# Kernel tuning notes

Hardware: AMD Instinct MI355X
Metric: run time of the kernel (lower is better)

## Reference

```python
import jax, jax.numpy as jnp
import numpy as np

R_RAYS = 65536
S_PER_RAY = 128
N_TOTAL = R_RAYS * S_PER_RAY


def setup_inputs() -> dict:
    key = jax.random.key(0)
    k1, k2, k3, k4 = jax.random.split(key, 4)
    sigmas = jax.random.uniform(k1, (N_TOTAL,), dtype=jnp.float32) * 2.0  # densities >= 0
    rgbs = jax.random.uniform(k2, (N_TOTAL, 3), dtype=jnp.float32)
    deltas = jax.random.uniform(k3, (N_TOTAL,), dtype=jnp.float32) * 0.01 + 1e-3
    ts = jax.random.uniform(k4, (N_TOTAL,), dtype=jnp.float32) * 6.0 + 0.1
    ray_idx = jnp.arange(R_RAYS, dtype=jnp.int32)
    rays_a = jnp.stack([ray_idx, ray_idx * S_PER_RAY,
                        jnp.full((R_RAYS,), S_PER_RAY, dtype=jnp.int32)], axis=1)
    return {"sigmas": sigmas, "rgbs": rgbs, "deltas": deltas, "ts": ts,
            "rays_a": rays_a, "T_threshold": 1e-4}


def reference(sigmas, rgbs, deltas, ts, rays_a, T_threshold):
    R = rays_a.shape[0]
    N = sigmas.shape[0]
    S_max = int(jnp.max(rays_a[:, 2]))  # max samples per ray (concrete)

    offs = jnp.arange(S_max, dtype=rays_a.dtype)
    valid = offs[None, :] < rays_a[:, 2, None]              # [R, S] prefix mask
    idx = jnp.where(valid, rays_a[:, 1, None] + offs[None, :], N - 1)  # [R, S]

    a = 1.0 - jnp.exp(-sigmas[idx] * deltas[idx])           # [R, S] alphas

    # Sequential transmittance recurrence with early-exit (T set to 0 once below threshold)
    def step(T, xs):
        a_s, v_s = xs                                        # [R], [R]
        alive = (T > T_threshold) & v_s
        w = jnp.where(alive, a_s * T, 0.0)
        T = jnp.where(alive, T * (1.0 - a_s), 0.0)
        return T, (w, alive)

    T0 = jnp.ones((R,), sigmas.dtype)
    _, (wT, aliveT) = jax.lax.scan(step, T0, (a.T, valid.T))
    w = wT.T                                                 # [R, S] weights
    alive = aliveT.T

    op_n = jnp.sum(w, axis=1)                                # [R]
    dep_n = jnp.sum(w * ts[idx], axis=1)                     # [R]
    rgb_n = jnp.einsum('rs,rsc->rc', w, rgbs[idx])           # [R, 3]
    cnt_n = jnp.sum(alive, axis=1).astype(jnp.int32)

    ridx = rays_a[:, 0]
    opacity = jnp.zeros((R,), w.dtype).at[ridx].add(op_n)
    depth = jnp.zeros((R,), w.dtype).at[ridx].add(dep_n)
    rgb = jnp.zeros((R, 3), w.dtype).at[ridx].add(rgb_n)
    total_samples = jnp.zeros((R,), jnp.int32).at[ridx].add(cnt_n)
    # invalid slots were mapped to index N-1 with w=0, so .add is safe
    ws = jnp.zeros((N,), w.dtype).at[idx.reshape(-1)].add(w.reshape(-1))

    return total_samples.sum(), opacity, depth, rgb, ws
```

## Files before the change

### kernel.cpp

```cpp
#include <hip/hip_runtime.h>


typedef float f4a __attribute__((ext_vector_type(4), aligned(4)));

template<int CTRL, int RM>
__device__ __forceinline__ float dpp_mul1(float v) {
    float t = __int_as_float(__builtin_amdgcn_update_dpp(
        0x3f800000, __float_as_int(v), CTRL, RM, 0xF, false));
    return v * t;
}
template<int CTRL>
__device__ __forceinline__ float dpp_add0(float v) {
    float t = __int_as_float(__builtin_amdgcn_update_dpp(
        0, __float_as_int(v), CTRL, 0xF, 0xF, false));
    return v + t;
}
__device__ __forceinline__ float seg_reduce32(float v) {
    v = dpp_add0<0x101>(v);
    v = dpp_add0<0x102>(v);
    v = dpp_add0<0x104>(v);
    v = dpp_add0<0x108>(v);
    v += __int_as_float(__builtin_amdgcn_ds_swizzle(
            __float_as_int(v), 0x401F));
    return v;
}

__global__ __launch_bounds__(256) void vr_main(
    const float* __restrict__ sigmas, const float* __restrict__ rgbs,
    const float* __restrict__ deltas, const float* __restrict__ ts,
    const int* __restrict__ rays_a, const float* __restrict__ thr_p,
    float* __restrict__ out, float* __restrict__ cnt_ws,
    int R, int use_ws)
{
    __shared__ float lds[4][2][384];

    const int wib  = (int)(threadIdx.x >> 6);
    const int wid  = (int)blockIdx.x * 4 + wib;
    const int lane = (int)(threadIdx.x & 63);
    const int half = lane >> 5;
    const int sl   = lane & 31;
    const int ray  = 2 * wid + half;
    const bool inR = ray < R;

    int ridx = 0, start = 0, count = 0;
    if (inR) {
        ridx  = rays_a[3 * ray + 0];
        start = rays_a[3 * ray + 1];
        count = rays_a[3 * ray + 2];
    }
    const float thr = thr_p[0];

    const bool ok = inR && (count == 128) && ((start & 3) == 0);
    const bool fastw = __all(ok);

    float fe[4], tv[4], rr[4], gg[4], bb[4];
    bool  v[4];

    if (fastw) {
        const float4 sg4 = *(const float4*)(sigmas + start + 4 * sl);
        const float4 dt4 = *(const float4*)(deltas + start + 4 * sl);
        const float4 tt4 = *(const float4*)(ts     + start + 4 * sl);

        const float4* rg = (const float4*)(rgbs + 3 * (size_t)start);
        float* L = &lds[wib][half][0];
        #pragma unroll
        for (int j = 0; j < 3; ++j) {
            float4 c = rg[32 * j + sl];
            *(float4*)(L + 128 * j + 4 * sl) = c;
        }
        fe[0] = __expf(-sg4.x * dt4.x);
        fe[1] = __expf(-sg4.y * dt4.y);
        fe[2] = __expf(-sg4.z * dt4.z);
        fe[3] = __expf(-sg4.w * dt4.w);
        tv[0] = tt4.x; tv[1] = tt4.y; tv[2] = tt4.z; tv[3] = tt4.w;

        asm volatile("s_waitcnt lgkmcnt(0)" ::: "memory");
        const float4 c0 = *(const float4*)(L + 12 * sl + 0);
        const float4 c1 = *(const float4*)(L + 12 * sl + 4);
        const float4 c2 = *(const float4*)(L + 12 * sl + 8);
        rr[0] = c0.x; rr[1] = c0.w; rr[2] = c1.z; rr[3] = c2.y;
        gg[0] = c0.y; gg[1] = c1.x; gg[2] = c1.w; gg[3] = c2.z;
        bb[0] = c0.z; bb[1] = c1.y; bb[2] = c2.x; bb[3] = c2.w;
        v[0] = v[1] = v[2] = v[3] = true;
    } else {
        #pragma unroll
        for (int i = 0; i < 4; ++i) {
            const int s = 4 * sl + i;
            const bool vi = inR && (s < count);
            v[i] = vi;
            float sg = 0.f, dt = 0.f;
            tv[i] = 0.f; rr[i] = 0.f; gg[i] = 0.f; bb[i] = 0.f;
            if (vi) {
                sg = sigmas[start + s];
                dt = deltas[start + s];
                tv[i] = ts[start + s];
                const float* rg = rgbs + 3 * ((size_t)start + s);
                rr[i] = rg[0]; gg[i] = rg[1]; bb[i] = rg[2];
            }
            fe[i] = vi ? __expf(-sg * dt) : 1.f;
        }
    }

    const float fprod = (fe[0] * fe[1]) * (fe[2] * fe[3]);
    float inc = fprod;
    inc = dpp_mul1<0x111, 0xF>(inc);
    inc = dpp_mul1<0x112, 0xF>(inc);
    inc = dpp_mul1<0x114, 0xF>(inc);
    inc = dpp_mul1<0x118, 0xF>(inc);
    inc = dpp_mul1<0x142, 0xA>(inc);

    float T = inc / fprod;

    float w[4];
    float cnt = 0.f;
    #pragma unroll
    for (int i = 0; i < 4; ++i) {
        const bool alive = v[i] && (T > thr);
        const float Tn = T * fe[i];
        w[i] = alive ? (T - Tn) : 0.f;
        cnt += alive ? 1.f : 0.f;
        T = Tn;
    }

    float* wsp = out + 1 + 5 * (size_t)R + (size_t)start + 4 * sl;
    if (fastw) {
        f4a wv; wv.x = w[0]; wv.y = w[1]; wv.z = w[2]; wv.w = w[3];
        *(f4a*)wsp = wv;
    } else {
        #pragma unroll
        for (int i = 0; i < 4; ++i) if (v[i]) wsp[i] = w[i];
    }

    float op  = (w[0] + w[1]) + (w[2] + w[3]);
    float dep = fmaf(w[0], tv[0], fmaf(w[1], tv[1], fmaf(w[2], tv[2], w[3] * tv[3])));
    float cr  = fmaf(w[0], rr[0], fmaf(w[1], rr[1], fmaf(w[2], rr[2], w[3] * rr[3])));
    float cg  = fmaf(w[0], gg[0], fmaf(w[1], gg[1], fmaf(w[2], gg[2], w[3] * gg[3])));
    float cb  = fmaf(w[0], bb[0], fmaf(w[1], bb[1], fmaf(w[2], bb[2], w[3] * bb[3])));

    op  = seg_reduce32(op);
    dep = seg_reduce32(dep);
    cr  = seg_reduce32(cr);
    cg  = seg_reduce32(cg);
    cb  = seg_reduce32(cb);
    cnt = seg_reduce32(cnt);

    if (sl == 0 && inR) {
        out[1 + ridx]             = op;
        out[1 + R + ridx]         = dep;
        out[1 + 2*R + 3*ridx + 0] = cr;
        out[1 + 2*R + 3*ridx + 1] = cg;
        out[1 + 2*R + 3*ridx + 2] = cb;
        if (use_ws) cnt_ws[ray] = cnt;
        else        atomicAdd(&out[0], cnt);
    }
}

__global__ __launch_bounds__(1024) void vr_total(
    const float* __restrict__ cnt_ws, float* __restrict__ out, int R)
{
    __shared__ float sm[16];
    float s = 0.f;
    const int R4 = R & ~3;
    for (int i = (int)threadIdx.x * 4; i < R4; i += 4096) {
        const float4 c = *(const float4*)(cnt_ws + i);
        s += (c.x + c.y) + (c.z + c.w);
    }
    if (threadIdx.x == 0)
        for (int i = R4; i < R; ++i) s += cnt_ws[i];
    #pragma unroll
    for (int d = 32; d; d >>= 1) s += __shfl_xor(s, d, 64);
    if ((threadIdx.x & 63) == 0) sm[threadIdx.x >> 6] = s;
    __syncthreads();
    if (threadIdx.x == 0) {
        float t = 0.f;
        #pragma unroll
        for (int k = 0; k < 16; ++k) t += sm[k];
        out[0] = t;
    }
}

extern "C" void kernel_launch(void* const* d_in, const int* in_sizes, int n_in,
                              void* d_out, int out_size, void* d_ws, size_t ws_size,
                              hipStream_t stream) {
    const float* sigmas = (const float*)d_in[0];
    const float* rgbs   = (const float*)d_in[1];
    const float* deltas = (const float*)d_in[2];
    const float* ts     = (const float*)d_in[3];
    const int*   rays_a = (const int*)d_in[4];
    const float* thr    = (const float*)d_in[5];
    int R = in_sizes[4] / 3;
    float* out = (float*)d_out;
    float* cnt_ws = (float*)d_ws;

    int use_ws = (ws_size >= (size_t)R * sizeof(float)) ? 1 : 0;

    if (!use_ws)
        hipMemsetAsync(d_out, 0, 4, stream);

    int grid = (R + 7) / 8;
    vr_main<<<grid, 256, 0, stream>>>(sigmas, rgbs, deltas, ts, rays_a, thr,
                                      out, cnt_ws, R, use_ws);
    if (use_ws)
        vr_total<<<1, 1024, 0, stream>>>(cnt_ws, out, R);
}
```

Before: 46.59 us.

## Replace count workspace and second kernel with per-block atomic; load rgb directly

The sample count is now reduced per block through shared memory and added to the output with one atomicAdd per block. This replaces the per-ray workspace write and the separate single-block total kernel, removing a kernel launch and its serial tail in exchange for a memset and contended atomics. The RGB data is now read with three float4 global loads per lane instead of being staged through LDS. The weight store becomes nontemporal.

```diff
diff --git a/kernel.cpp b/kernel.cpp
--- a/kernel.cpp
+++ b/kernel.cpp
@@ -1,7 +1,5 @@
 #include <hip/hip_runtime.h>
 
-
-typedef float f4a __attribute__((ext_vector_type(4), aligned(4)));
 
 template<int CTRL, int RM>
 __device__ __forceinline__ float dpp_mul1(float v) {
@@ -25,14 +23,15 @@
     return v;
 }
 
+typedef float f4a __attribute__((ext_vector_type(4), aligned(4)));
+
 __global__ __launch_bounds__(256) void vr_main(
     const float* __restrict__ sigmas, const float* __restrict__ rgbs,
     const float* __restrict__ deltas, const float* __restrict__ ts,
     const int* __restrict__ rays_a, const float* __restrict__ thr_p,
-    float* __restrict__ out, float* __restrict__ cnt_ws,
-    int R, int use_ws)
+    float* __restrict__ out, int R)
 {
-    __shared__ float lds[4][2][384];
+    __shared__ float blksum[4];
 
     const int wib  = (int)(threadIdx.x >> 6);
     const int wid  = (int)blockIdx.x * 4 + wib;
@@ -60,27 +59,20 @@
         const float4 sg4 = *(const float4*)(sigmas + start + 4 * sl);
         const float4 dt4 = *(const float4*)(deltas + start + 4 * sl);
         const float4 tt4 = *(const float4*)(ts     + start + 4 * sl);
+        const float* rg = rgbs + 3 * ((size_t)start + 4 * sl);
+        const float4 c0 = *(const float4*)(rg + 0);
+        const float4 c1 = *(const float4*)(rg + 4);
+        const float4 c2 = *(const float4*)(rg + 8);
 
-        const float4* rg = (const float4*)(rgbs + 3 * (size_t)start);
-        float* L = &lds[wib][half][0];
-        #pragma unroll
-        for (int j = 0; j < 3; ++j) {
-            float4 c = rg[32 * j + sl];
-            *(float4*)(L + 128 * j + 4 * sl) = c;
-        }
         fe[0] = __expf(-sg4.x * dt4.x);
         fe[1] = __expf(-sg4.y * dt4.y);
         fe[2] = __expf(-sg4.z * dt4.z);
         fe[3] = __expf(-sg4.w * dt4.w);
         tv[0] = tt4.x; tv[1] = tt4.y; tv[2] = tt4.z; tv[3] = tt4.w;
-
-        asm volatile("s_waitcnt lgkmcnt(0)" ::: "memory");
-        const float4 c0 = *(const float4*)(L + 12 * sl + 0);
-        const float4 c1 = *(const float4*)(L + 12 * sl + 4);
-        const float4 c2 = *(const float4*)(L + 12 * sl + 8);
-        rr[0] = c0.x; rr[1] = c0.w; rr[2] = c1.z; rr[3] = c2.y;
-        gg[0] = c0.y; gg[1] = c1.x; gg[2] = c1.w; gg[3] = c2.z;
-        bb[0] = c0.z; bb[1] = c1.y; bb[2] = c2.x; bb[3] = c2.w;
+        rr[0] = c0.x; gg[0] = c0.y; bb[0] = c0.z;
+        rr[1] = c0.w; gg[1] = c1.x; bb[1] = c1.y;
+        rr[2] = c1.z; gg[2] = c1.w; bb[2] = c2.x;
+        rr[3] = c2.y; gg[3] = c2.z; bb[3] = c2.w;
         v[0] = v[1] = v[2] = v[3] = true;
     } else {
         #pragma unroll
@@ -125,7 +117,7 @@
     float* wsp = out + 1 + 5 * (size_t)R + (size_t)start + 4 * sl;
     if (fastw) {
         f4a wv; wv.x = w[0]; wv.y = w[1]; wv.z = w[2]; wv.w = w[3];
-        *(f4a*)wsp = wv;
+        __builtin_nontemporal_store(wv, (f4a*)wsp);
     } else {
         #pragma unroll
         for (int i = 0; i < 4; ++i) if (v[i]) wsp[i] = w[i];
@@ -142,7 +134,6 @@
     cr  = seg_reduce32(cr);
     cg  = seg_reduce32(cg);
     cb  = seg_reduce32(cb);
-    cnt = seg_reduce32(cnt);
 
     if (sl == 0 && inR) {
         out[1 + ridx]             = op;
@@ -150,32 +141,15 @@
         out[1 + 2*R + 3*ridx + 0] = cr;
         out[1 + 2*R + 3*ridx + 1] = cg;
         out[1 + 2*R + 3*ridx + 2] = cb;
-        if (use_ws) cnt_ws[ray] = cnt;
-        else        atomicAdd(&out[0], cnt);
     }
-}
 
-__global__ __launch_bounds__(1024) void vr_total(
-    const float* __restrict__ cnt_ws, float* __restrict__ out, int R)
-{
-    __shared__ float sm[16];
-    float s = 0.f;
-    const int R4 = R & ~3;
-    for (int i = (int)threadIdx.x * 4; i < R4; i += 4096) {
-        const float4 c = *(const float4*)(cnt_ws + i);
-        s += (c.x + c.y) + (c.z + c.w);
-    }
-    if (threadIdx.x == 0)
-        for (int i = R4; i < R; ++i) s += cnt_ws[i];
-    #pragma unroll
-    for (int d = 32; d; d >>= 1) s += __shfl_xor(s, d, 64);
-    if ((threadIdx.x & 63) == 0) sm[threadIdx.x >> 6] = s;
+    cnt = seg_reduce32(cnt);
+    cnt += __shfl_xor(cnt, 32, 64);
+    if (lane == 0) blksum[wib] = cnt;
     __syncthreads();
     if (threadIdx.x == 0) {
-        float t = 0.f;
-        #pragma unroll
-        for (int k = 0; k < 16; ++k) t += sm[k];
-        out[0] = t;
+        float t = (blksum[0] + blksum[1]) + (blksum[2] + blksum[3]);
+        atomicAdd(&out[0], t);
     }
 }
 
@@ -190,16 +164,10 @@
     const float* thr    = (const float*)d_in[5];
     int R = in_sizes[4] / 3;
     float* out = (float*)d_out;
-    float* cnt_ws = (float*)d_ws;
 
-    int use_ws = (ws_size >= (size_t)R * sizeof(float)) ? 1 : 0;
-
-    if (!use_ws)
-        hipMemsetAsync(d_out, 0, 4, stream);
+    hipMemsetAsync(d_out, 0, 4, stream);
 
     int grid = (R + 7) / 8;
     vr_main<<<grid, 256, 0, stream>>>(sigmas, rgbs, deltas, ts, rays_a, thr,
-                                      out, cnt_ws, R, use_ws);
-    if (use_ws)
-        vr_total<<<1, 1024, 0, stream>>>(cnt_ws, out, R);
+                                      out, R);
 }
```

Measured after the change: 122.5 us. 2.63x slower.
